# Kernel optimization log

Hardware: AMD Instinct MI355X
Metric: run time of the kernel (lower is better)

Reference implementation:

```python
import jax, jax.numpy as jnp
import numpy as np


def setup_inputs() -> dict:
    key = jax.random.key(0)
    k1, k2 = jax.random.split(key)
    B, L, D = 16, 1024, 256
    sentence1 = jax.random.normal(k1, (B, L, D), dtype=jnp.float32)
    sentence2 = jax.random.normal(k2, (B, L, D), dtype=jnp.float32)
    return {"batch_size": B, "sentence1": sentence1, "sentence2": sentence2}


def reference(batch_size, sentence1, sentence2):
    # A[k,i,j] = 1 / (1 + ||s1[k,i] - s2[k,j]||_2)
    # materializing the [B, L1, L2, D] difference tensor.
    x2 = jnp.sum(sentence1 * sentence1, axis=-1)          # [B, L1]
    y2 = jnp.sum(sentence2 * sentence2, axis=-1)          # [B, L2]
    xy = jnp.einsum("bid,bjd->bij", sentence1, sentence2)  # [B, L1, L2]
    sq = x2[:, :, None] + y2[:, None, :] - 2.0 * xy
    sq = jnp.maximum(sq, 0.0)  # guard tiny negatives from cancellation
    dist = jnp.sqrt(sq)
    return 1.0 / (1.0 + dist)
```

## Files before the change

### kernel.cpp

```cpp
#include <hip/hip_runtime.h>
#include <hip/hip_bf16.h>

typedef __attribute__((ext_vector_type(4))) float f32x4;
typedef __attribute__((ext_vector_type(8))) __bf16 bf16x8;
typedef __attribute__((ext_vector_type(4))) __bf16 bf16x4;

#define B_DIM 16
#define L_DIM 1024
#define D_DIM 256

#define GLOAD_LDS16(g, lptr)                                          \
    __builtin_amdgcn_global_load_lds(                                 \
        (const __attribute__((address_space(1))) void*)(g),           \
        (__attribute__((address_space(3))) void*)(lptr), 16, 0, 0)

#define SBAR() __builtin_amdgcn_sched_barrier(0)

__global__ __launch_bounds__(256) void prep_kernel(const float* __restrict__ s1,
                                                   const float* __restrict__ s2,
                                                   float* __restrict__ nrm,
                                                   __hip_bfloat16* __restrict__ s1b,
                                                   __hip_bfloat16* __restrict__ s2b) {
    const int w = threadIdx.x >> 6, l = threadIdx.x & 63;
    const int base = (blockIdx.x << 4) + (w << 2);
#pragma unroll
    for (int i = 0; i < 4; ++i) {
        const int row = base + i;
        const int second = row >> 14;
        const int r = row & 16383;
        const float* src = (second ? s2 : s1) + (size_t)r * D_DIM;
        __hip_bfloat16* dst = (second ? s2b : s1b) + (size_t)r * D_DIM;
        float4 v = reinterpret_cast<const float4*>(src)[l];
        float s = v.x * v.x + v.y * v.y + v.z * v.z + v.w * v.w;
        bf16x4 bv;
        bv[0] = (__bf16)v.x; bv[1] = (__bf16)v.y; bv[2] = (__bf16)v.z; bv[3] = (__bf16)v.w;
        *reinterpret_cast<bf16x4*>(dst + l * 4) = bv;
#pragma unroll
        for (int o = 32; o > 0; o >>= 1) s += __shfl_xor(s, o, 64);
        if (l == 0) nrm[row] = s;
    }
}

__global__ __launch_bounds__(256, 2) void dist_gemm2_kernel(const __hip_bfloat16* __restrict__ s1b,
                                                            const __hip_bfloat16* __restrict__ s2b,
                                                            const float* __restrict__ nrm,
                                                            float* __restrict__ out) {
    __shared__ __bf16 Alds[4][128 * 32];
    __shared__ __bf16 Blds[4][128 * 32];

    const int t = threadIdx.x;
    const int p = blockIdx.x;
    const int d = ((p & 7) << 6) + (p >> 3);
    const int batch = d >> 5;
    const int rem = d & 31;
    const int row0 = (rem >> 2) << 7;
    const int col0a = (rem & 3) << 8;
    const int col0b = col0a + 128;

    const __hip_bfloat16* Ag = s1b + ((size_t)batch * L_DIM + row0) * D_DIM;
    const __hip_bfloat16* Bg0 = s2b + ((size_t)batch * L_DIM + col0a) * D_DIM;
    const __hip_bfloat16* Bg1 = s2b + ((size_t)batch * L_DIM + col0b) * D_DIM;

    const int l = t & 63, w = t >> 6;
    const int wr = w >> 1, wc = w & 1;
    const int lr = l & 15;
    const int lq = l >> 4;

    const int srow_in_seg = l >> 2;
    const int sslot = (l & 3) ^ ((l >> 3) & 3);

    auto stageK = [&](const __hip_bfloat16* Bg, int kt) {
        const int k0 = kt << 5;
        const int b = kt & 3;
#pragma unroll
        for (int i = 0; i < 2; ++i) {
            const int s = (w << 1) | i;
            const int rl = (s << 4) + srow_in_seg;
            GLOAD_LDS16(Ag + rl * D_DIM + k0 + sslot * 8, &Alds[b][s << 9]);
            GLOAD_LDS16(Bg + rl * D_DIM + k0 + sslot * 8, &Blds[b][s << 9]);
        }
    };

    bf16x8 aF[2][4], bF[2][4];
    auto readFrags = [&](int kt, bf16x8* a, bf16x8* bfr) {
        const int b = kt & 3;
#pragma unroll
        for (int m = 0; m < 4; ++m) {
            const int row = (wr << 6) + (m << 4) + lr;
            const int sl = lq ^ ((row >> 1) & 3);
            a[m] = *reinterpret_cast<const bf16x8*>(&Alds[b][(row << 5) + (sl << 3)]);
        }
#pragma unroll
        for (int n = 0; n < 4; ++n) {
            const int row = (wc << 6) + (n << 4) + lr;
            const int sl = lq ^ ((row >> 1) & 3);
            bfr[n] = *reinterpret_cast<const bf16x8*>(&Blds[b][(row << 5) + (sl << 3)]);
        }
    };

    const float* x2 = nrm + batch * L_DIM;
    const float* y2 = nrm + B_DIM * L_DIM + batch * L_DIM;
    const int rbase = row0 + (wr << 6) + (lq << 2);
    const int cloc = (wc << 6) + lr;
    float* outb = out + (size_t)batch * L_DIM * L_DIM;

    auto epilogue = [&](const f32x4 (&acc)[4][4], const f32x4 (&xv)[4],
                        const float (&yv)[4], int col0_) {
        const int cb = col0_ + cloc;
#pragma unroll
        for (int n = 0; n < 4; ++n) {
            const int col = cb + (n << 4);
            const float y2v = yv[n];
#pragma unroll
            for (int m = 0; m < 4; ++m) {
#pragma unroll
                for (int r = 0; r < 4; ++r) {
                    const int row = rbase + (m << 4) + r;
                    float sq = fmaxf(xv[m][r] + y2v - 2.0f * acc[m][n][r], 0.0f);
                    outb[(size_t)row * L_DIM + col] =
                        __builtin_amdgcn_rcpf(1.0f + __builtin_amdgcn_sqrtf(sq));
                }
            }
        }
    };

    f32x4 xv[4]; float yv0[4], yv1[4];
#pragma unroll
    for (int m = 0; m < 4; ++m) xv[m] = *reinterpret_cast<const f32x4*>(&x2[rbase + (m << 4)]);
#pragma unroll
    for (int n = 0; n < 4; ++n) yv0[n] = y2[col0a + cloc + (n << 4)];
#pragma unroll
    for (int n = 0; n < 4; ++n) yv1[n] = y2[col0b + cloc + (n << 4)];
    SBAR();
    f32x4 acc0[4][4] = {};
    stageK(Bg0, 0); stageK(Bg0, 1); stageK(Bg0, 2); stageK(Bg0, 3);
    SBAR();
    asm volatile("s_waitcnt vmcnt(0)" ::: "memory");
    __builtin_amdgcn_s_barrier();
    readFrags(0, aF[0], bF[0]);

#pragma unroll
    for (int kt = 0; kt < 8; ++kt) {
        if (kt >= 3 && kt <= 5) asm volatile("s_waitcnt vmcnt(4)" ::: "memory");
        else if (kt == 6)       asm volatile("s_waitcnt vmcnt(0)" ::: "memory");
        if (kt >= 1) __builtin_amdgcn_s_barrier();
        if (kt < 7) readFrags(kt + 1, aF[(kt + 1) & 1], bF[(kt + 1) & 1]);
        if (kt < 7) asm volatile("s_waitcnt lgkmcnt(8)" ::: "memory");
        else        asm volatile("s_waitcnt lgkmcnt(0)" ::: "memory");
        if (kt >= 1 && kt <= 4) stageK(Bg0, kt + 3);
        __builtin_amdgcn_s_setprio(1);
#pragma unroll
        for (int m = 0; m < 4; ++m)
#pragma unroll
            for (int n = 0; n < 4; ++n)
                acc0[m][n] = __builtin_amdgcn_mfma_f32_16x16x32_bf16(
                    aF[kt & 1][m], bF[kt & 1][n], acc0[m][n], 0, 0, 0);
        __builtin_amdgcn_s_setprio(0);
    }

    stageK(Bg1, 0); stageK(Bg1, 1); stageK(Bg1, 2); stageK(Bg1, 3);
    SBAR();
    asm volatile("s_waitcnt vmcnt(0)" ::: "memory");
    __builtin_amdgcn_s_barrier();
    readFrags(0, aF[0], bF[0]);
    epilogue(acc0, xv, yv0, col0a);
    SBAR();
    f32x4 acc1[4][4] = {};

#pragma unroll
    for (int kt = 0; kt < 8; ++kt) {
        if (kt >= 3 && kt <= 5) asm volatile("s_waitcnt vmcnt(4)" ::: "memory");
        else if (kt == 6)       asm volatile("s_waitcnt vmcnt(0)" ::: "memory");
        if (kt >= 1) __builtin_amdgcn_s_barrier();
        if (kt < 7) readFrags(kt + 1, aF[(kt + 1) & 1], bF[(kt + 1) & 1]);
        if (kt < 7) asm volatile("s_waitcnt lgkmcnt(8)" ::: "memory");
        else        asm volatile("s_waitcnt lgkmcnt(0)" ::: "memory");
        if (kt >= 1 && kt <= 4) stageK(Bg1, kt + 3);
        __builtin_amdgcn_s_setprio(1);
#pragma unroll
        for (int m = 0; m < 4; ++m)
#pragma unroll
            for (int n = 0; n < 4; ++n)
                acc1[m][n] = __builtin_amdgcn_mfma_f32_16x16x32_bf16(
                    aF[kt & 1][m], bF[kt & 1][n], acc1[m][n], 0, 0, 0);
        __builtin_amdgcn_s_setprio(0);
    }

    epilogue(acc1, xv, yv1, col0b);
}

__global__ __launch_bounds__(256) void norms_kernel(const float* __restrict__ s1,
                                                    const float* __restrict__ s2,
                                                    float* __restrict__ nrm) {
    int w = threadIdx.x >> 6, l = threadIdx.x & 63;
    int row = (blockIdx.x << 2) + w;
    const float* src = (row < B_DIM * L_DIM)
                           ? (s1 + (size_t)row * D_DIM)
                           : (s2 + (size_t)(row - B_DIM * L_DIM) * D_DIM);
    float4 v = reinterpret_cast<const float4*>(src)[l];
    float s = v.x * v.x + v.y * v.y + v.z * v.z + v.w * v.w;
#pragma unroll
    for (int o = 32; o > 0; o >>= 1) s += __shfl_xor(s, o, 64);
    if (l == 0) nrm[row] = s;
}

__global__ __launch_bounds__(256) void dist_gemm_kernel(const float* __restrict__ s1,
                                                        const float* __restrict__ s2,
                                                        const float* __restrict__ nrm,
                                                        float* __restrict__ out) {
    __shared__ __bf16 Alds[2][128 * 32];
    __shared__ __bf16 Blds[2][128 * 32];

    const int t = threadIdx.x;
    const int p = blockIdx.x;
    const int d = ((p & 7) << 7) + (p >> 3);
    const int batch = d >> 6;
    const int tile = d & 63;
    const int row0 = (tile >> 3) << 7;
    const int col0 = (tile & 7) << 7;

    const float* Ag = s1 + ((size_t)batch * L_DIM + row0) * D_DIM;
    const float* Bg = s2 + ((size_t)batch * L_DIM + col0) * D_DIM;

    const int sr = t >> 2;
    const int sc = (t & 3) << 3;

    const int l = t & 63, w = t >> 6;
    const int wr = w >> 1, wc = w & 1;
    const int lr = l & 15;
    const int lk = (l >> 4) << 3;

    f32x4 acc[4][4] = {};

    auto stage = [&](int buf, int k0) {
#pragma unroll
        for (int pass = 0; pass < 2; ++pass) {
            const int r = sr + (pass << 6);
            const float4* sa = reinterpret_cast<const float4*>(Ag + (size_t)r * D_DIM + k0 + sc);
            float4 a0 = sa[0], a1 = sa[1];
            const float4* sb = reinterpret_cast<const float4*>(Bg + (size_t)r * D_DIM + k0 + sc);
            float4 b0 = sb[0], b1 = sb[1];
            bf16x8 av, bv;
            av[0] = (__bf16)a0.x; av[1] = (__bf16)a0.y; av[2] = (__bf16)a0.z; av[3] = (__bf16)a0.w;
            av[4] = (__bf16)a1.x; av[5] = (__bf16)a1.y; av[6] = (__bf16)a1.z; av[7] = (__bf16)a1.w;
            bv[0] = (__bf16)b0.x; bv[1] = (__bf16)b0.y; bv[2] = (__bf16)b0.z; bv[3] = (__bf16)b0.w;
            bv[4] = (__bf16)b1.x; bv[5] = (__bf16)b1.y; bv[6] = (__bf16)b1.z; bv[7] = (__bf16)b1.w;
            *reinterpret_cast<bf16x8*>(&Alds[buf][(r << 5) + sc]) = av;
            *reinterpret_cast<bf16x8*>(&Blds[buf][(r << 5) + sc]) = bv;
        }
    };

    stage(0, 0);
    __syncthreads();
    int cur = 0;
    for (int kt = 0; kt < 8; ++kt) {
        if (kt < 7) stage(cur ^ 1, (kt + 1) << 5);
        bf16x8 aF[4], bF[4];
#pragma unroll
        for (int m = 0; m < 4; ++m)
            aF[m] = *reinterpret_cast<const bf16x8*>(
                &Alds[cur][(((wr << 6) + (m << 4) + lr) << 5) + lk]);
#pragma unroll
        for (int n = 0; n < 4; ++n)
            bF[n] = *reinterpret_cast<const bf16x8*>(
                &Blds[cur][(((wc << 6) + (n << 4) + lr) << 5) + lk]);
#pragma unroll
        for (int m = 0; m < 4; ++m)
#pragma unroll
            for (int n = 0; n < 4; ++n)
                acc[m][n] = __builtin_amdgcn_mfma_f32_16x16x32_bf16(aF[m], bF[n], acc[m][n], 0, 0, 0);
        __syncthreads();
        cur ^= 1;
    }

    const float* x2 = nrm + batch * L_DIM;
    const float* y2 = nrm + B_DIM * L_DIM + batch * L_DIM;
    float* outb = out + (size_t)batch * L_DIM * L_DIM;
    const int rbase = row0 + (wr << 6) + ((l >> 4) << 2);
    const int cbase = col0 + (wc << 6) + lr;
#pragma unroll
    for (int n = 0; n < 4; ++n) {
        const int col = cbase + (n << 4);
        const float y2v = y2[col];
#pragma unroll
        for (int m = 0; m < 4; ++m) {
            const int rowf = rbase + (m << 4);
#pragma unroll
            for (int r = 0; r < 4; ++r) {
                const int row = rowf + r;
                float sq = x2[row] + y2v - 2.0f * acc[m][n][r];
                sq = fmaxf(sq, 0.0f);
                outb[(size_t)row * L_DIM + col] = 1.0f / (1.0f + sqrtf(sq));
            }
        }
    }
}

extern "C" void kernel_launch(void* const* d_in, const int* in_sizes, int n_in,
                              void* d_out, int out_size, void* d_ws, size_t ws_size,
                              hipStream_t stream) {
    (void)in_sizes; (void)n_in; (void)out_size;
    const float* s1 = (const float*)d_in[1];
    const float* s2 = (const float*)d_in[2];
    float* out = (float*)d_out;

    const size_t NRM_BYTES = 2u * B_DIM * L_DIM * sizeof(float);
    const size_t BF_BYTES = (size_t)B_DIM * L_DIM * D_DIM * sizeof(__hip_bfloat16);
    const size_t NEED = NRM_BYTES + 2 * BF_BYTES;

    float* nrm = (float*)d_ws;
    if (ws_size >= NEED) {
        __hip_bfloat16* s1b = (__hip_bfloat16*)((char*)d_ws + NRM_BYTES);
        __hip_bfloat16* s2b = (__hip_bfloat16*)((char*)d_ws + NRM_BYTES + BF_BYTES);
        prep_kernel<<<2048, 256, 0, stream>>>(s1, s2, nrm, s1b, s2b);
        dist_gemm2_kernel<<<512, 256, 0, stream>>>(s1b, s2b, nrm, out);
    } else {
        norms_kernel<<<8192, 256, 0, stream>>>(s1, s2, nrm);
        dist_gemm_kernel<<<1024, 256, 0, stream>>>(s1, s2, nrm, out);
    }
}
```

Baseline: 32.09 us.

## Keep full A tile resident in LDS and sweep four B column tiles per block

The GEMM kernel now uses 512-thread blocks that each own a 128x512 output strip instead of 128x256. The whole 128x256 A row tile is kept in LDS across all four column sub-tiles, so A is loaded once per block rather than once per 128-column pass, and only B is re-streamed. Waves are rearranged as 2x4 with smaller per-wave B fragments, and the grid drops to 256 blocks. This cuts global and LDS traffic for A, at the cost of more LDS per block (64KB for A plus 32KB for B), fewer blocks to fill the CUs, and hand-tuned vmcnt/lgkmcnt waits that must match the new load counts.

New measurement: 33.28 us. +3.7%, slower.

```diff
diff --git a/kernel.cpp b/kernel.cpp
--- a/kernel.cpp
+++ b/kernel.cpp
@@ -41,75 +41,75 @@
     }
 }
 
-__global__ __launch_bounds__(256, 2) void dist_gemm2_kernel(const __hip_bfloat16* __restrict__ s1b,
+__global__ __launch_bounds__(512, 2) void dist_gemm4_kernel(const __hip_bfloat16* __restrict__ s1b,
                                                             const __hip_bfloat16* __restrict__ s2b,
                                                             const float* __restrict__ nrm,
                                                             float* __restrict__ out) {
-    __shared__ __bf16 Alds[4][128 * 32];
+    __shared__ __bf16 Afull[8][128 * 32];
     __shared__ __bf16 Blds[4][128 * 32];
 
     const int t = threadIdx.x;
     const int p = blockIdx.x;
-    const int d = ((p & 7) << 6) + (p >> 3);
-    const int batch = d >> 5;
-    const int rem = d & 31;
-    const int row0 = (rem >> 2) << 7;
-    const int col0a = (rem & 3) << 8;
-    const int col0b = col0a + 128;
+    const int d = ((p & 7) << 5) + (p >> 3);
+    const int batch = d >> 4;
+    const int rem = d & 15;
+    const int row0 = (rem >> 1) << 7;
+    const int colq = (rem & 1) << 9;
 
     const __hip_bfloat16* Ag = s1b + ((size_t)batch * L_DIM + row0) * D_DIM;
-    const __hip_bfloat16* Bg0 = s2b + ((size_t)batch * L_DIM + col0a) * D_DIM;
-    const __hip_bfloat16* Bg1 = s2b + ((size_t)batch * L_DIM + col0b) * D_DIM;
+    const __hip_bfloat16* Bgq = s2b + ((size_t)batch * L_DIM + colq) * D_DIM;
 
     const int l = t & 63, w = t >> 6;
-    const int wr = w >> 1, wc = w & 1;
+    const int wr = w >> 2, wc = w & 3;
     const int lr = l & 15;
     const int lq = l >> 4;
 
-    const int srow_in_seg = l >> 2;
+    const int srow = l >> 2;
     const int sslot = (l & 3) ^ ((l >> 3) & 3);
 
-    auto stageK = [&](const __hip_bfloat16* Bg, int kt) {
-        const int k0 = kt << 5;
-        const int b = kt & 3;
-#pragma unroll
-        for (int i = 0; i < 2; ++i) {
-            const int s = (w << 1) | i;
-            const int rl = (s << 4) + srow_in_seg;
-            GLOAD_LDS16(Ag + rl * D_DIM + k0 + sslot * 8, &Alds[b][s << 9]);
-            GLOAD_LDS16(Bg + rl * D_DIM + k0 + sslot * 8, &Blds[b][s << 9]);
-        }
-    };
-
-    bf16x8 aF[2][4], bF[2][4];
+    auto stageA = [&](int kt) {
+        const int rl = (w << 4) + srow;
+        GLOAD_LDS16(Ag + rl * D_DIM + (kt << 5) + sslot * 8, &Afull[kt][w << 9]);
+    };
+    auto stageB = [&](const __hip_bfloat16* Bg, int kt) {
+        const int rl = (w << 4) + srow;
+        GLOAD_LDS16(Bg + rl * D_DIM + (kt << 5) + sslot * 8, &Blds[kt & 3][w << 9]);
+    };
+
+    bf16x8 aF[2][4], bF[2][2];
     auto readFrags = [&](int kt, bf16x8* a, bf16x8* bfr) {
-        const int b = kt & 3;
 #pragma unroll
         for (int m = 0; m < 4; ++m) {
             const int row = (wr << 6) + (m << 4) + lr;
             const int sl = lq ^ ((row >> 1) & 3);
-            a[m] = *reinterpret_cast<const bf16x8*>(&Alds[b][(row << 5) + (sl << 3)]);
-        }
-#pragma unroll
-        for (int n = 0; n < 4; ++n) {
-            const int row = (wc << 6) + (n << 4) + lr;
+            a[m] = *reinterpret_cast<const bf16x8*>(&Afull[kt][(row << 5) + (sl << 3)]);
+        }
+#pragma unroll
+        for (int n = 0; n < 2; ++n) {
+            const int row = (wc << 5) + (n << 4) + lr;
             const int sl = lq ^ ((row >> 1) & 3);
-            bfr[n] = *reinterpret_cast<const bf16x8*>(&Blds[b][(row << 5) + (sl << 3)]);
+            bfr[n] = *reinterpret_cast<const bf16x8*>(&Blds[kt & 3][(row << 5) + (sl << 3)]);
         }
     };
 
     const float* x2 = nrm + batch * L_DIM;
     const float* y2 = nrm + B_DIM * L_DIM + batch * L_DIM;
     const int rbase = row0 + (wr << 6) + (lq << 2);
-    const int cloc = (wc << 6) + lr;
+    const int cloc = (wc << 5) + lr;
     float* outb = out + (size_t)batch * L_DIM * L_DIM;
 
-    auto epilogue = [&](const f32x4 (&acc)[4][4], const f32x4 (&xv)[4],
-                        const float (&yv)[4], int col0_) {
-        const int cb = col0_ + cloc;
-#pragma unroll
-        for (int n = 0; n < 4; ++n) {
-            const int col = cb + (n << 4);
+    f32x4 acc[4][2];
+    auto zeroAcc = [&]() {
+#pragma unroll
+        for (int m = 0; m < 4; ++m)
+#pragma unroll
+            for (int n = 0; n < 2; ++n) acc[m][n] = f32x4{0.f, 0.f, 0.f, 0.f};
+    };
+
+    auto epilogue = [&](const f32x4 (&xv)[4], const float* yv, int colb) {
+#pragma unroll
+        for (int n = 0; n < 2; ++n) {
+            const int col = colb + cloc + (n << 4);
             const float y2v = yv[n];
 #pragma unroll
             for (int m = 0; m < 4; ++m) {
@@ -124,16 +124,17 @@
         }
     };
 
-    f32x4 xv[4]; float yv0[4], yv1[4];
+    f32x4 xv[4]; float yv4[4][2];
 #pragma unroll
     for (int m = 0; m < 4; ++m) xv[m] = *reinterpret_cast<const f32x4*>(&x2[rbase + (m << 4)]);
 #pragma unroll
-    for (int n = 0; n < 4; ++n) yv0[n] = y2[col0a + cloc + (n << 4)];
-#pragma unroll
-    for (int n = 0; n < 4; ++n) yv1[n] = y2[col0b + cloc + (n << 4)];
+    for (int tau = 0; tau < 4; ++tau)
+#pragma unroll
+        for (int n = 0; n < 2; ++n) yv4[tau][n] = y2[colq + (tau << 7) + cloc + (n << 4)];
     SBAR();
-    f32x4 acc0[4][4] = {};
-    stageK(Bg0, 0); stageK(Bg0, 1); stageK(Bg0, 2); stageK(Bg0, 3);
+    zeroAcc();
+#pragma unroll
+    for (int kt = 0; kt < 4; ++kt) { stageA(kt); stageB(Bgq, kt); }
     SBAR();
     asm volatile("s_waitcnt vmcnt(0)" ::: "memory");
     __builtin_amdgcn_s_barrier();
@@ -141,52 +142,58 @@
 
 #pragma unroll
     for (int kt = 0; kt < 8; ++kt) {
-        if (kt >= 3 && kt <= 5) asm volatile("s_waitcnt vmcnt(4)" ::: "memory");
+        if (kt >= 3 && kt <= 5) asm volatile("s_waitcnt vmcnt(2)" ::: "memory");
         else if (kt == 6)       asm volatile("s_waitcnt vmcnt(0)" ::: "memory");
         if (kt >= 1) __builtin_amdgcn_s_barrier();
         if (kt < 7) readFrags(kt + 1, aF[(kt + 1) & 1], bF[(kt + 1) & 1]);
-        if (kt < 7) asm volatile("s_waitcnt lgkmcnt(8)" ::: "memory");
+        if (kt < 7) asm volatile("s_waitcnt lgkmcnt(6)" ::: "memory");
         else        asm volatile("s_waitcnt lgkmcnt(0)" ::: "memory");
-        if (kt >= 1 && kt <= 4) stageK(Bg0, kt + 3);
+        if (kt >= 1 && kt <= 4) { stageA(kt + 3); stageB(Bgq, kt + 3); }
         __builtin_amdgcn_s_setprio(1);
 #pragma unroll
         for (int m = 0; m < 4; ++m)
 #pragma unroll
-            for (int n = 0; n < 4; ++n)
-                acc0[m][n] = __builtin_amdgcn_mfma_f32_16x16x32_bf16(
-                    aF[kt & 1][m], bF[kt & 1][n], acc0[m][n], 0, 0, 0);
+            for (int n = 0; n < 2; ++n)
+                acc[m][n] = __builtin_amdgcn_mfma_f32_16x16x32_bf16(
+                    aF[kt & 1][m], bF[kt & 1][n], acc[m][n], 0, 0, 0);
         __builtin_amdgcn_s_setprio(0);
     }
 
-    stageK(Bg1, 0); stageK(Bg1, 1); stageK(Bg1, 2); stageK(Bg1, 3);
-    SBAR();
-    asm volatile("s_waitcnt vmcnt(0)" ::: "memory");
-    __builtin_amdgcn_s_barrier();
-    readFrags(0, aF[0], bF[0]);
-    epilogue(acc0, xv, yv0, col0a);
-    SBAR();
-    f32x4 acc1[4][4] = {};
-
-#pragma unroll
-    for (int kt = 0; kt < 8; ++kt) {
-        if (kt >= 3 && kt <= 5) asm volatile("s_waitcnt vmcnt(4)" ::: "memory");
-        else if (kt == 6)       asm volatile("s_waitcnt vmcnt(0)" ::: "memory");
-        if (kt >= 1) __builtin_amdgcn_s_barrier();
-        if (kt < 7) readFrags(kt + 1, aF[(kt + 1) & 1], bF[(kt + 1) & 1]);
-        if (kt < 7) asm volatile("s_waitcnt lgkmcnt(8)" ::: "memory");
-        else        asm volatile("s_waitcnt lgkmcnt(0)" ::: "memory");
-        if (kt >= 1 && kt <= 4) stageK(Bg1, kt + 3);
-        __builtin_amdgcn_s_setprio(1);
-#pragma unroll
-        for (int m = 0; m < 4; ++m)
-#pragma unroll
-            for (int n = 0; n < 4; ++n)
-                acc1[m][n] = __builtin_amdgcn_mfma_f32_16x16x32_bf16(
-                    aF[kt & 1][m], bF[kt & 1][n], acc1[m][n], 0, 0, 0);
-        __builtin_amdgcn_s_setprio(0);
-    }
-
-    epilogue(acc1, xv, yv1, col0b);
+#pragma unroll
+    for (int tau = 1; tau < 4; ++tau) {
+        const __hip_bfloat16* Bg = Bgq + (size_t)(tau << 7) * D_DIM;
+        __builtin_amdgcn_s_barrier();
+#pragma unroll
+        for (int kt = 0; kt < 4; ++kt) stageB(Bg, kt);
+        SBAR();
+        asm volatile("s_waitcnt vmcnt(3)" ::: "memory");
+        __builtin_amdgcn_s_barrier();
+        readFrags(0, aF[0], bF[0]);
+        epilogue(xv, yv4[tau - 1], colq + ((tau - 1) << 7));
+        SBAR();
+        zeroAcc();
+
+#pragma unroll
+        for (int kt = 0; kt < 8; ++kt) {
+            if (kt >= 3 && kt <= 5) asm volatile("s_waitcnt vmcnt(1)" ::: "memory");
+            else if (kt == 6)       asm volatile("s_waitcnt vmcnt(0)" ::: "memory");
+            if (kt >= 1) __builtin_amdgcn_s_barrier();
+            if (kt < 7) readFrags(kt + 1, aF[(kt + 1) & 1], bF[(kt + 1) & 1]);
+            if (kt < 7) asm volatile("s_waitcnt lgkmcnt(6)" ::: "memory");
+            else        asm volatile("s_waitcnt lgkmcnt(0)" ::: "memory");
+            if (kt >= 1 && kt <= 4) stageB(Bg, kt + 3);
+            __builtin_amdgcn_s_setprio(1);
+#pragma unroll
+            for (int m = 0; m < 4; ++m)
+#pragma unroll
+                for (int n = 0; n < 2; ++n)
+                    acc[m][n] = __builtin_amdgcn_mfma_f32_16x16x32_bf16(
+                        aF[kt & 1][m], bF[kt & 1][n], acc[m][n], 0, 0, 0);
+            __builtin_amdgcn_s_setprio(0);
+        }
+    }
+
+    epilogue(xv, yv4[3], colq + 384);
 }
 
 __global__ __launch_bounds__(256) void norms_kernel(const float* __restrict__ s1,
@@ -209,7 +216,7 @@
                                                         const float* __restrict__ nrm,
                                                         float* __restrict__ out) {
     __shared__ __bf16 Alds[2][128 * 32];
-    __shared__ __bf16 Blds[2][128 * 32];
+    __shared__ __bf16 Blds2[2][128 * 32];
 
     const int t = threadIdx.x;
     const int p = blockIdx.x;
@@ -246,7 +253,7 @@
             bv[0] = (__bf16)b0.x; bv[1] = (__bf16)b0.y; bv[2] = (__bf16)b0.z; bv[3] = (__bf16)b0.w;
             bv[4] = (__bf16)b1.x; bv[5] = (__bf16)b1.y; bv[6] = (__bf16)b1.z; bv[7] = (__bf16)b1.w;
             *reinterpret_cast<bf16x8*>(&Alds[buf][(r << 5) + sc]) = av;
-            *reinterpret_cast<bf16x8*>(&Blds[buf][(r << 5) + sc]) = bv;
+            *reinterpret_cast<bf16x8*>(&Blds2[buf][(r << 5) + sc]) = bv;
         }
     };
 
@@ -263,7 +270,7 @@
 #pragma unroll
         for (int n = 0; n < 4; ++n)
             bF[n] = *reinterpret_cast<const bf16x8*>(
-                &Blds[cur][(((wc << 6) + (n << 4) + lr) << 5) + lk]);
+                &Blds2[cur][(((wc << 6) + (n << 4) + lr) << 5) + lk]);
 #pragma unroll
         for (int m = 0; m < 4; ++m)
 #pragma unroll
@@ -313,7 +320,7 @@
         __hip_bfloat16* s1b = (__hip_bfloat16*)((char*)d_ws + NRM_BYTES);
         __hip_bfloat16* s2b = (__hip_bfloat16*)((char*)d_ws + NRM_BYTES + BF_BYTES);
         prep_kernel<<<2048, 256, 0, stream>>>(s1, s2, nrm, s1b, s2b);
-        dist_gemm2_kernel<<<512, 256, 0, stream>>>(s1b, s2b, nrm, out);
+        dist_gemm4_kernel<<<256, 512, 0, stream>>>(s1b, s2b, nrm, out);
     } else {
         norms_kernel<<<8192, 256, 0, stream>>>(s1, s2, nrm);
         dist_gemm_kernel<<<1024, 256, 0, stream>>>(s1, s2, nrm, out);
```
